# Kernel optimization log

Measured on AMD Instinct MI355X. Metric: run time of the kernel, lower is better.

## Reference

```python
import jax, jax.numpy as jnp
import numpy as np

NUM_HEADS = 16
D_MODEL = 1024
D_K = 64
D_V = 64
NEG_INF = -1e9


def setup_inputs() -> dict:
    key = jax.random.key(0)
    ks = jax.random.split(key, 7)
    B, S = 2, 2048
    Q = jax.random.normal(ks[0], (B, S, D_MODEL), dtype=jnp.float32)
    K = jax.random.normal(ks[1], (B, S, D_MODEL), dtype=jnp.float32)
    V = jax.random.normal(ks[2], (B, S, D_MODEL), dtype=jnp.float32)
    s = 1.0 / np.sqrt(D_MODEL)
    W_q = jax.random.normal(ks[3], (D_MODEL, D_K * NUM_HEADS), dtype=jnp.float32) * s
    W_k = jax.random.normal(ks[4], (D_MODEL, D_K), dtype=jnp.float32) * s
    W_v = jax.random.normal(ks[5], (D_MODEL, D_V), dtype=jnp.float32) * s
    W_o = jax.random.normal(ks[6], (D_V * NUM_HEADS, D_MODEL), dtype=jnp.float32) * (1.0 / np.sqrt(D_V * NUM_HEADS))
    return {"Q": Q, "K": K, "V": V, "W_q": W_q, "W_k": W_k, "W_v": W_v, "W_o": W_o}


def reference(Q, K, V, W_q, W_k, W_v, W_o):
    B, Sq, _ = Q.shape
    Sk = K.shape[1]
    # projections: Q -> per-head, K/V -> single shared head (MQA)
    q = (Q @ W_q).reshape(B, Sq, NUM_HEADS, D_K).transpose(0, 2, 1, 3)  # [B,H,Sq,Dk]
    k = K @ W_k  # [B,Sk,Dk]
    v = V @ W_v  # [B,Sk,Dv]
    scores = jnp.einsum('bhqd,bkd->bhqk', q, k) / jnp.sqrt(jnp.float32(D_K))
    causal = jnp.tril(jnp.ones((Sq, Sk), dtype=bool))  # [Sq,Sk]
    scores = jnp.where(causal[None, None], scores, NEG_INF)
    attn = jax.nn.softmax(scores, axis=-1)  # [B,H,Sq,Sk]
    out = jnp.einsum('bhqk,bkd->bhqd', attn, v)  # [B,H,Sq,Dv]
    out = out.transpose(0, 2, 1, 3).reshape(B, Sq, NUM_HEADS * D_V)
    return out @ W_o
```

## Files before the change

### kernel.cpp

```cpp
#include <hip/hip_runtime.h>
#include <hip/hip_bf16.h>
#include <cstdint>

typedef __bf16 bf16_t;
typedef __bf16 bf16x8 __attribute__((ext_vector_type(8)));
typedef __bf16 bf16x4 __attribute__((ext_vector_type(4)));
typedef float  floatx4 __attribute__((ext_vector_type(4)));

__device__ __forceinline__ bf16_t f2bf(float x) { return (bf16_t)x; }

__device__ __forceinline__ void gll16(const void* g, void* l) {
  __builtin_amdgcn_global_load_lds((const __attribute__((address_space(1))) void*)g,
                                   (__attribute__((address_space(3))) void*)l, 16, 0, 0);
}

#define S_LEN 2048
#define NHEAD 16

__global__ __launch_bounds__(256) void prep_all(const float* __restrict__ Wq,
                                                const float* __restrict__ Wo,
                                                const float* __restrict__ Wk,
                                                const float* __restrict__ Wv,
                                                const float* __restrict__ Q,
                                                bf16_t* __restrict__ Wqt,
                                                bf16_t* __restrict__ Wot,
                                                bf16_t* __restrict__ Wkt,
                                                bf16_t* __restrict__ Wvt,
                                                bf16_t* __restrict__ Qb) {
  const int bid = blockIdx.x;
  if (bid >= 2176) {
    const int base = (bid - 2176) * 8192;
#pragma unroll
    for (int j = 0; j < 8; ++j) {
      int idx = base + j * 1024 + threadIdx.x * 4;
      float4 v = *(const float4*)(Q + idx);
      bf16x4 o;
      o[0] = f2bf(v.x); o[1] = f2bf(v.y); o[2] = f2bf(v.z); o[3] = f2bf(v.w);
      *(bf16x4*)(Qb + idx) = o;
    }
    return;
  }
  const float* W; bf16_t* Wt; int n0, k0, N;
  if (bid < 2048) {
    int z = bid >> 10, rem = bid & 1023;
    W = z ? Wo : Wq; Wt = z ? Wot : Wqt;
    n0 = (rem & 31) * 32; k0 = (rem >> 5) * 32; N = 1024;
  } else {
    int b2 = bid - 2048, z = b2 >> 6, rem = b2 & 63;
    W = z ? Wv : Wk; Wt = z ? Wvt : Wkt;
    n0 = (rem & 1) * 32; k0 = (rem >> 1) * 32; N = 64;
  }
  const int K = 1024;
  __shared__ float tile[32][33];
  int tx = threadIdx.x & 31, ty = threadIdx.x >> 5;
#pragma unroll
  for (int r = 0; r < 4; ++r)
    tile[ty + 8 * r][tx] = W[(size_t)(k0 + ty + 8 * r) * N + n0 + tx];
  __syncthreads();
#pragma unroll
  for (int r = 0; r < 4; ++r)
    Wt[(size_t)(n0 + ty + 8 * r) * K + k0 + tx] = f2bf(tile[tx][ty + 8 * r]);
}

template <int OUTMODE>
__device__ __forceinline__ void gemm64_body(const bf16_t* __restrict__ A,
                                            const bf16_t* __restrict__ Bt,
                                            void* __restrict__ Cout,
                                            int M, int N, int K,
                                            int m0, int n0,
                                            bf16_t* As, bf16_t* Bs) {
  const int tid = threadIdx.x;
  const int wave = tid >> 6, lane = tid & 63;
  const int quad = lane >> 4, lm = lane & 15;
  const int wr = wave >> 1, wc = wave & 1;

  floatx4 acc[2][2];
#pragma unroll
  for (int i = 0; i < 2; ++i)
#pragma unroll
    for (int j = 0; j < 2; ++j) acc[i][j] = (floatx4){0.f, 0.f, 0.f, 0.f};

  for (int k0 = 0; k0 < K; k0 += 64) {
#pragma unroll
    for (int rd = 0; rd < 2; ++rd) {
      int idx = rd * 256 + tid, row = idx >> 3, ch = (idx & 7) ^ (row & 7);
      gll16(A + (size_t)(m0 + row) * K + k0 + ch * 8,
            As + (rd * 256 + wave * 64) * 8);
    }
#pragma unroll
    for (int rd = 0; rd < 2; ++rd) {
      int idx = rd * 256 + tid, row = idx >> 3, ch = (idx & 7) ^ (row & 7);
      gll16(Bt + (size_t)(n0 + row) * K + k0 + ch * 8,
            Bs + (rd * 256 + wave * 64) * 8);
    }
    __syncthreads();
    const int sw = lm & 7;
    bf16x8 af[2][2], bfr[2][2];
#pragma unroll
    for (int i = 0; i < 2; ++i) {
      const bf16_t* base = &As[(wr * 32 + i * 16 + lm) * 64];
      af[i][0] = *(const bf16x8*)(base + ((quad ^ sw) * 8));
      af[i][1] = *(const bf16x8*)(base + (((4 + quad) ^ sw) * 8));
    }
#pragma unroll
    for (int j = 0; j < 2; ++j) {
      const bf16_t* base = &Bs[(wc * 32 + j * 16 + lm) * 64];
      bfr[j][0] = *(const bf16x8*)(base + ((quad ^ sw) * 8));
      bfr[j][1] = *(const bf16x8*)(base + (((4 + quad) ^ sw) * 8));
    }
#pragma unroll
    for (int ks = 0; ks < 2; ++ks)
#pragma unroll
      for (int i = 0; i < 2; ++i)
#pragma unroll
        for (int j = 0; j < 2; ++j)
          acc[i][j] = __builtin_amdgcn_mfma_f32_16x16x32_bf16(af[i][ks], bfr[j][ks],
                                                              acc[i][j], 0, 0, 0);
    __syncthreads();
  }
#pragma unroll
  for (int i = 0; i < 2; ++i) {
#pragma unroll
    for (int j = 0; j < 2; ++j) {
      int row0 = m0 + wr * 32 + i * 16 + quad * 4;
      int col = n0 + wc * 32 + j * 16 + lm;
#pragma unroll
      for (int r = 0; r < 4; ++r) {
        if constexpr (OUTMODE == 3)
          ((bf16_t*)Cout)[(size_t)(row0 + r) * N + col] = f2bf(acc[i][j][r] * 0.125f);
        else
          ((float*)Cout)[(size_t)(row0 + r) * N + col] = acc[i][j][r];
      }
    }
  }
}

__device__ __forceinline__ void kv_body(const float* __restrict__ A32,
                                        const bf16_t* __restrict__ Bt,
                                        bf16_t* __restrict__ kp,
                                        bf16_t* __restrict__ vpt,
                                        int M, int K, int m0, int isV,
                                        bf16_t* As, bf16_t* Bs) {
  constexpr int BK = 32, LDK = 40, N = 64;
  const int tid = threadIdx.x;
  const int wave = tid >> 6, lane = tid & 63;
  const int quad = lane >> 4, lm = lane & 15;
  const int wr = wave >> 1, wc = wave & 1;

  floatx4 acc[2][2];
#pragma unroll
  for (int i = 0; i < 2; ++i)
#pragma unroll
    for (int j = 0; j < 2; ++j) acc[i][j] = (floatx4){0.f, 0.f, 0.f, 0.f};

  for (int k0 = 0; k0 < K; k0 += BK) {
    {
      int row = tid >> 2, c8 = tid & 3;
      const float* src = A32 + (size_t)(m0 + row) * K + k0 + c8 * 8;
      float4 f0 = *(const float4*)src;
      float4 f1 = *(const float4*)(src + 4);
      bf16x8 o;
      o[0] = f2bf(f0.x); o[1] = f2bf(f0.y); o[2] = f2bf(f0.z); o[3] = f2bf(f0.w);
      o[4] = f2bf(f1.x); o[5] = f2bf(f1.y); o[6] = f2bf(f1.z); o[7] = f2bf(f1.w);
      *(bf16x8*)&As[row * LDK + c8 * 8] = o;
    }
    {
      int row = tid >> 2, c8 = tid & 3;
      *(bf16x8*)&Bs[row * LDK + c8 * 8] =
          *(const bf16x8*)(Bt + (size_t)row * K + k0 + c8 * 8);
    }
    __syncthreads();
    bf16x8 af[2], bfr[2];
#pragma unroll
    for (int i = 0; i < 2; ++i)
      af[i] = *(const bf16x8*)&As[(wr * 32 + i * 16 + lm) * LDK + quad * 8];
#pragma unroll
    for (int j = 0; j < 2; ++j)
      bfr[j] = *(const bf16x8*)&Bs[(wc * 32 + j * 16 + lm) * LDK + quad * 8];
#pragma unroll
    for (int i = 0; i < 2; ++i)
#pragma unroll
      for (int j = 0; j < 2; ++j)
        acc[i][j] = __builtin_amdgcn_mfma_f32_16x16x32_bf16(af[i], bfr[j],
                                                            acc[i][j], 0, 0, 0);
    __syncthreads();
  }
#pragma unroll
  for (int i = 0; i < 2; ++i) {
#pragma unroll
    for (int j = 0; j < 2; ++j) {
      int row0 = m0 + wr * 32 + i * 16 + quad * 4;
      int col = wc * 32 + j * 16 + lm;
      if (isV) {
        bf16x4 o;
#pragma unroll
        for (int r = 0; r < 4; ++r) o[r] = f2bf(acc[i][j][r]);
        *(bf16x4*)&vpt[(size_t)col * M + row0] = o;
      } else {
#pragma unroll
        for (int r = 0; r < 4; ++r)
          kp[(size_t)(row0 + r) * N + col] = f2bf(acc[i][j][r]);
      }
    }
  }
}

__global__ __launch_bounds__(256, 4) void proj_all(const bf16_t* __restrict__ Qb,
                                                   const float* __restrict__ K,
                                                   const float* __restrict__ V,
                                                   const bf16_t* __restrict__ Wqt,
                                                   const bf16_t* __restrict__ Wkt,
                                                   const bf16_t* __restrict__ Wvt,
                                                   bf16_t* __restrict__ qp,
                                                   bf16_t* __restrict__ kp,
                                                   bf16_t* __restrict__ vpt,
                                                   int BS) {
  __shared__ __align__(16) bf16_t As[64 * 64];
  __shared__ __align__(16) bf16_t Bs[64 * 64];
  const int bid = blockIdx.x;
  const int mB = BS / 64;
  const int nQ = mB * 16;
  if (bid < nQ) {
    int m0 = (bid % mB) * 64, n0 = (bid / mB) * 64;
    gemm64_body<3>(Qb, Wqt, qp, BS, 1024, 1024, m0, n0, As, Bs);
  } else {
    int b2 = bid - nQ;
    int isV = (b2 >= mB);
    int m0 = (b2 % mB) * 64;
    kv_body(isV ? V : K, isV ? Wvt : Wkt, kp, vpt, BS, 1024, m0, isV, As, Bs);
  }
}

__global__ __launch_bounds__(256, 4) void gemm_oproj(const bf16_t* __restrict__ A,
                                                     const bf16_t* __restrict__ Bt,
                                                     float* __restrict__ Cout,
                                                     int M, int N, int K) {
  __shared__ __align__(16) bf16_t As[64 * 64];
  __shared__ __align__(16) bf16_t Bs[64 * 64];
  gemm64_body<0>(A, Bt, Cout, M, N, K, blockIdx.x * 64, blockIdx.y * 64, As, Bs);
}

__global__ __launch_bounds__(256, 2) void flash_mqa(const bf16_t* __restrict__ q,
                                                    const bf16_t* __restrict__ kk,
                                                    const bf16_t* __restrict__ vt,
                                                    bf16_t* __restrict__ Opart,
                                                    float* __restrict__ lpart,
                                                    int BStot) {
  const int c = blockIdx.x;
  int qt, s;
  if (c < 16)      { qt = c; s = 0; }
  else if (c < 48) { qt = 16 + ((c - 16) >> 1); s = (c - 16) & 1; }
  else if (c < 96) { int d = c - 48; int q3 = d / 3; qt = 32 + q3; s = d - q3 * 3; }
  else             { qt = 48 + ((c - 96) >> 2); s = (c - 96) & 3; }
  const int n = (qt >> 1) + 1;
  const int nchunks = (n + 7) >> 3;
  const int kt0 = s * 8;
  const int kt1 = (kt0 + 8 < n) ? kt0 + 8 : n;
  const int ktmax = n - 1;

  const int hg = blockIdx.y, b = blockIdx.z;
  const int tid = threadIdx.x;
  const int wave = tid >> 6, lane = tid & 63;
  const int quad = lane >> 4, lm = lane & 15;
  const int h = hg * 4 + wave;

  __shared__ __align__(16) bf16_t k_lds[2][64 * 64];
  __shared__ __align__(16) bf16_t v_lds[2][64 * 64];
  __shared__ __align__(16) bf16_t p_lds[4][32 * 64];

  const size_t bS = (size_t)b * S_LEN;
  const int qb = qt * 32;
  const int qoff = qb - ktmax * 64;
  const int sw = lm & 7;

  bf16x8 qf[2][2];
#pragma unroll
  for (int m = 0; m < 2; ++m) {
    const bf16_t* qp = q + (bS + qb + m * 16 + lm) * 1024 + h * 64;
    qf[m][0] = *(const bf16x8*)(qp + quad * 8);
    qf[m][1] = *(const bf16x8*)(qp + 32 + quad * 8);
  }
  bf16x8 onesf;
#pragma unroll
  for (int j = 0; j < 8; ++j) onesf[j] = f2bf(1.0f);

  floatx4 acc[2][4];
  floatx4 ps[2];
#pragma unroll
  for (int m = 0; m < 2; ++m) {
    ps[m] = (floatx4){0.f, 0.f, 0.f, 0.f};
#pragma unroll
    for (int t = 0; t < 4; ++t) acc[m][t] = (floatx4){0.f, 0.f, 0.f, 0.f};
  }

  bf16x8 kst[2], vst[2];
  auto load_kv = [&](int kt) {
    const int k0 = kt * 64;
#pragma unroll
    for (int it = 0; it < 2; ++it) {
      int idx = it * 256 + tid, r = idx >> 3, c8 = idx & 7;
      kst[it] = *(const bf16x8*)(kk + (bS + k0 + r) * 64 + c8 * 8);
      vst[it] = *(const bf16x8*)(vt + (size_t)r * BStot + bS + k0 + c8 * 8);
    }
  };
  auto write_kv = [&](int buf) {
#pragma unroll
    for (int it = 0; it < 2; ++it) {
      int idx = it * 256 + tid, r = idx >> 3, c8 = idx & 7;
      int addr = r * 64 + ((c8 ^ (r & 7)) * 8);
      *(bf16x8*)&k_lds[buf][addr] = kst[it];
      *(bf16x8*)&v_lds[buf][addr] = vst[it];
    }
  };

  load_kv(kt0);
  write_kv(kt0 & 1);
  __syncthreads();

  for (int kt = kt0; kt < kt1; ++kt) {
    const int cur = kt & 1;
    if (kt + 1 < kt1) load_kv(kt + 1);
    const bool diag = (kt == ktmax);

#pragma unroll
    for (int t = 0; t < 4; ++t) {
      const bf16_t* kb = &k_lds[cur][(t * 16 + lm) * 64];
      bf16x8 a0 = *(const bf16x8*)(kb + ((quad ^ sw) * 8));
      bf16x8 a1 = *(const bf16x8*)(kb + (((4 + quad) ^ sw) * 8));
      floatx4 sv[2];
#pragma unroll
      for (int m = 0; m < 2; ++m) {
        floatx4 cc = (floatx4){0.f, 0.f, 0.f, 0.f};
        cc = __builtin_amdgcn_mfma_f32_16x16x32_bf16(a0, qf[m][0], cc, 0, 0, 0);
        cc = __builtin_amdgcn_mfma_f32_16x16x32_bf16(a1, qf[m][1], cc, 0, 0, 0);
        sv[m] = cc;
      }
      if (diag) {
#pragma unroll
        for (int m = 0; m < 2; ++m) {
          int qq = qoff + m * 16 + lm;
#pragma unroll
          for (int r = 0; r < 4; ++r) {
            int kj = t * 16 + quad * 4 + r;
            sv[m][r] = (kj <= qq) ? __expf(sv[m][r]) : 0.f;
          }
        }
      } else {
#pragma unroll
        for (int m = 0; m < 2; ++m)
#pragma unroll
          for (int r = 0; r < 4; ++r) sv[m][r] = __expf(sv[m][r]);
      }
#pragma unroll
      for (int m = 0; m < 2; ++m) {
        bf16x4 pk;
#pragma unroll
        for (int r = 0; r < 4; ++r) pk[r] = f2bf(sv[m][r]);
        *(bf16x4*)&p_lds[wave][(m * 16 + lm) * 64 +
                               (((2 * t + (quad >> 1)) ^ sw) * 8) + (quad & 1) * 4] = pk;
      }
    }
    bf16x8 p0[2], p1[2];
#pragma unroll
    for (int m = 0; m < 2; ++m) {
      const bf16_t* pb = &p_lds[wave][(m * 16 + lm) * 64];
      p0[m] = *(const bf16x8*)(pb + ((quad ^ sw) * 8));
      p1[m] = *(const bf16x8*)(pb + (((4 + quad) ^ sw) * 8));
      ps[m] = __builtin_amdgcn_mfma_f32_16x16x32_bf16(p0[m], onesf, ps[m], 0, 0, 0);
      ps[m] = __builtin_amdgcn_mfma_f32_16x16x32_bf16(p1[m], onesf, ps[m], 0, 0, 0);
    }
#pragma unroll
    for (int t = 0; t < 4; ++t) {
      const bf16_t* vb = &v_lds[cur][(t * 16 + lm) * 64];
      bf16x8 v0 = *(const bf16x8*)(vb + ((quad ^ sw) * 8));
      bf16x8 v1 = *(const bf16x8*)(vb + (((4 + quad) ^ sw) * 8));
#pragma unroll
      for (int m = 0; m < 2; ++m) {
        acc[m][t] = __builtin_amdgcn_mfma_f32_16x16x32_bf16(p0[m], v0, acc[m][t], 0, 0, 0);
        acc[m][t] = __builtin_amdgcn_mfma_f32_16x16x32_bf16(p1[m], v1, acc[m][t], 0, 0, 0);
      }
    }
    if (kt + 1 < kt1) write_kv(1 - cur);
    __syncthreads();
  }

  const size_t slotO = (size_t)BStot * 1024;
  const size_t slotL = (size_t)BStot * 16;
#pragma unroll
  for (int m = 0; m < 2; ++m) {
    const int q0 = qb + m * 16 + quad * 4;
#pragma unroll
    for (int t = 0; t < 4; ++t)
#pragma unroll
      for (int r = 0; r < 4; ++r)
        Opart[s * slotO + (bS + q0 + r) * 1024 + h * 64 + t * 16 + lm] =
            f2bf(acc[m][t][r]);
    if (lm == 0)
#pragma unroll
      for (int r = 0; r < 4; ++r)
        lpart[s * slotL + (bS + q0 + r) * 16 + h] = ps[m][r];
  }
  if (s == 0) {
    for (int ss = nchunks; ss < 4; ++ss) {
#pragma unroll
      for (int m = 0; m < 2; ++m) {
        const int q0 = qb + m * 16 + quad * 4;
#pragma unroll
        for (int t = 0; t < 4; ++t)
#pragma unroll
          for (int r = 0; r < 4; ++r)
            Opart[ss * slotO + (bS + q0 + r) * 1024 + h * 64 + t * 16 + lm] = f2bf(0.f);
        if (lm == 0)
#pragma unroll
          for (int r = 0; r < 4; ++r)
            lpart[ss * slotL + (bS + q0 + r) * 16 + h] = 0.f;
      }
    }
  }
}

__global__ __launch_bounds__(256) void combine_o(const bf16_t* __restrict__ Opart,
                                                 const float* __restrict__ lpart,
                                                 bf16_t* __restrict__ Ob, int BS) {
  const int idx = (blockIdx.x * 256 + threadIdx.x) * 8;
  const int row = idx >> 10, col = idx & 1023, h = col >> 6;
  const size_t slotO = (size_t)BS * 1024;
  const size_t slotL = (size_t)BS * 16;
  float l = 0.f;
#pragma unroll
  for (int s = 0; s < 4; ++s) l += lpart[s * slotL + row * 16 + h];
  float o[8];
#pragma unroll
  for (int j = 0; j < 8; ++j) o[j] = 0.f;
#pragma unroll
  for (int s = 0; s < 4; ++s) {
    bf16x8 v = *(const bf16x8*)(Opart + s * slotO + idx);
#pragma unroll
    for (int j = 0; j < 8; ++j) o[j] += (float)v[j];
  }
  const float rl = 1.0f / l;
  bf16x8 out;
#pragma unroll
  for (int j = 0; j < 8; ++j) out[j] = f2bf(o[j] * rl);
  *(bf16x8*)(Ob + idx) = out;
}

extern "C" void kernel_launch(void* const* d_in, const int* in_sizes, int n_in,
                              void* d_out, int out_size, void* d_ws, size_t ws_size,
                              hipStream_t stream) {
  const float* Q  = (const float*)d_in[0];
  const float* K  = (const float*)d_in[1];
  const float* V  = (const float*)d_in[2];
  const float* Wq = (const float*)d_in[3];
  const float* Wk = (const float*)d_in[4];
  const float* Wv = (const float*)d_in[5];
  const float* Wo = (const float*)d_in[6];

  const int BS = in_sizes[0] / 1024;
  const int B  = BS / S_LEN;

  bf16_t* ws  = (bf16_t*)d_ws;
  bf16_t* qp  = ws;
  bf16_t* Ob  = qp  + (size_t)BS * 1024;
  bf16_t* Wqt = Ob  + (size_t)BS * 1024;
  bf16_t* Wot = Wqt + (size_t)1024 * 1024;
  bf16_t* Wkt = Wot + (size_t)1024 * 1024;
  bf16_t* Wvt = Wkt + (size_t)64 * 1024;
  bf16_t* kp  = Wvt + (size_t)64 * 1024;
  bf16_t* vpt = kp  + (size_t)BS * 64;
  bf16_t* Opart = vpt + (size_t)BS * 64;
  float*  lpart = (float*)(Opart + (size_t)4 * BS * 1024);
  bf16_t* Qb  = (bf16_t*)(lpart + (size_t)4 * BS * 16);

  prep_all<<<2176 + BS / 8, 256, 0, stream>>>(Wq, Wo, Wk, Wv, Q,
                                              Wqt, Wot, Wkt, Wvt, Qb);

  proj_all<<<(BS / 64) * 16 + (BS / 64) * 2, 256, 0, stream>>>(
      Qb, K, V, Wqt, Wkt, Wvt, qp, kp, vpt, BS);

  flash_mqa<<<dim3(160, NHEAD / 4, B), 256, 0, stream>>>(qp, kp, vpt, Opart, lpart, BS);

  combine_o<<<(BS * 1024) / (256 * 8), 256, 0, stream>>>(Opart, lpart, Ob, BS);

  gemm_oproj<<<dim3(BS / 64, 16), 256, 0, stream>>>(Ob, Wot, (float*)d_out, BS, 1024, 1024);
}
```

Before: 194.0 us.

## Double-buffer GEMM tiles through registers and widen N tile to 128

```diff
diff --git a/kernel.cpp b/kernel.cpp
--- a/kernel.cpp
+++ b/kernel.cpp
@@ -8,11 +8,6 @@
 typedef float  floatx4 __attribute__((ext_vector_type(4)));
 
 __device__ __forceinline__ bf16_t f2bf(float x) { return (bf16_t)x; }
-
-__device__ __forceinline__ void gll16(const void* g, void* l) {
-  __builtin_amdgcn_global_load_lds((const __attribute__((address_space(1))) void*)g,
-                                   (__attribute__((address_space(3))) void*)l, 16, 0, 0);
-}
 
 #define S_LEN 2048
 #define NHEAD 16
@@ -63,48 +58,72 @@
 }
 
 template <int OUTMODE>
-__device__ __forceinline__ void gemm64_body(const bf16_t* __restrict__ A,
-                                            const bf16_t* __restrict__ Bt,
-                                            void* __restrict__ Cout,
-                                            int M, int N, int K,
-                                            int m0, int n0,
-                                            bf16_t* As, bf16_t* Bs) {
+__device__ __forceinline__ void gemm_body(const bf16_t* __restrict__ A,
+                                          const bf16_t* __restrict__ Bt,
+                                          void* __restrict__ Cout,
+                                          int M, int N, int K,
+                                          int m0, int n0,
+                                          bf16_t* As, bf16_t* Bs) {
   const int tid = threadIdx.x;
   const int wave = tid >> 6, lane = tid & 63;
   const int quad = lane >> 4, lm = lane & 15;
   const int wr = wave >> 1, wc = wave & 1;
-
-  floatx4 acc[2][2];
+  const int sw = lm & 7;
+
+  floatx4 acc[2][4];
 #pragma unroll
   for (int i = 0; i < 2; ++i)
 #pragma unroll
-    for (int j = 0; j < 2; ++j) acc[i][j] = (floatx4){0.f, 0.f, 0.f, 0.f};
-
-  for (int k0 = 0; k0 < K; k0 += 64) {
+    for (int j = 0; j < 4; ++j) acc[i][j] = (floatx4){0.f, 0.f, 0.f, 0.f};
+
+  const int nIter = K / 64;
+  const int phase = blockIdx.x & (nIter - 1);
+
+  bf16x8 ast[2], bst[4];
+  auto load_t = [&](int it) {
+    const int kk = ((it + phase) & (nIter - 1)) * 64;
 #pragma unroll
     for (int rd = 0; rd < 2; ++rd) {
-      int idx = rd * 256 + tid, row = idx >> 3, ch = (idx & 7) ^ (row & 7);
-      gll16(A + (size_t)(m0 + row) * K + k0 + ch * 8,
-            As + (rd * 256 + wave * 64) * 8);
-    }
+      int idx = rd * 256 + tid, row = idx >> 3, c8 = idx & 7;
+      ast[rd] = *(const bf16x8*)(A + (size_t)(m0 + row) * K + kk + c8 * 8);
+    }
+#pragma unroll
+    for (int rd = 0; rd < 4; ++rd) {
+      int idx = rd * 256 + tid, row = idx >> 3, c8 = idx & 7;
+      bst[rd] = *(const bf16x8*)(Bt + (size_t)(n0 + row) * K + kk + c8 * 8);
+    }
+  };
+  auto write_t = [&](int buf) {
 #pragma unroll
     for (int rd = 0; rd < 2; ++rd) {
-      int idx = rd * 256 + tid, row = idx >> 3, ch = (idx & 7) ^ (row & 7);
-      gll16(Bt + (size_t)(n0 + row) * K + k0 + ch * 8,
-            Bs + (rd * 256 + wave * 64) * 8);
-    }
-    __syncthreads();
-    const int sw = lm & 7;
-    bf16x8 af[2][2], bfr[2][2];
+      int idx = rd * 256 + tid, row = idx >> 3, c8 = idx & 7;
+      *(bf16x8*)&As[buf * 4096 + row * 64 + ((c8 ^ (row & 7)) * 8)] = ast[rd];
+    }
+#pragma unroll
+    for (int rd = 0; rd < 4; ++rd) {
+      int idx = rd * 256 + tid, row = idx >> 3, c8 = idx & 7;
+      *(bf16x8*)&Bs[buf * 8192 + row * 64 + ((c8 ^ (row & 7)) * 8)] = bst[rd];
+    }
+  };
+
+  load_t(0);
+  write_t(0);
+  __syncthreads();
+
+  for (int it = 0; it < nIter; ++it) {
+    const int cur = it & 1;
+    if (it + 1 < nIter) load_t(it + 1);
+
+    bf16x8 af[2][2], bfr[4][2];
 #pragma unroll
     for (int i = 0; i < 2; ++i) {
-      const bf16_t* base = &As[(wr * 32 + i * 16 + lm) * 64];
+      const bf16_t* base = &As[cur * 4096 + (wr * 32 + i * 16 + lm) * 64];
       af[i][0] = *(const bf16x8*)(base + ((quad ^ sw) * 8));
       af[i][1] = *(const bf16x8*)(base + (((4 + quad) ^ sw) * 8));
     }
 #pragma unroll
-    for (int j = 0; j < 2; ++j) {
-      const bf16_t* base = &Bs[(wc * 32 + j * 16 + lm) * 64];
+    for (int j = 0; j < 4; ++j) {
+      const bf16_t* base = &Bs[cur * 8192 + (wc * 64 + j * 16 + lm) * 64];
       bfr[j][0] = *(const bf16x8*)(base + ((quad ^ sw) * 8));
       bfr[j][1] = *(const bf16x8*)(base + (((4 + quad) ^ sw) * 8));
     }
@@ -113,17 +132,19 @@
 #pragma unroll
       for (int i = 0; i < 2; ++i)
 #pragma unroll
-        for (int j = 0; j < 2; ++j)
+        for (int j = 0; j < 4; ++j)
           acc[i][j] = __builtin_amdgcn_mfma_f32_16x16x32_bf16(af[i][ks], bfr[j][ks],
                                                               acc[i][j], 0, 0, 0);
+    if (it + 1 < nIter) write_t(1 - cur);
     __syncthreads();
   }
+
 #pragma unroll
   for (int i = 0; i < 2; ++i) {
 #pragma unroll
-    for (int j = 0; j < 2; ++j) {
+    for (int j = 0; j < 4; ++j) {
       int row0 = m0 + wr * 32 + i * 16 + quad * 4;
-      int col = n0 + wc * 32 + j * 16 + lm;
+      int col = n0 + wc * 64 + j * 16 + lm;
 #pragma unroll
       for (int r = 0; r < 4; ++r) {
         if constexpr (OUTMODE == 3)
@@ -205,7 +226,7 @@
   }
 }
 
-__global__ __launch_bounds__(256, 4) void proj_all(const bf16_t* __restrict__ Qb,
+__global__ __launch_bounds__(256, 3) void proj_all(const bf16_t* __restrict__ Qb,
                                                    const float* __restrict__ K,
                                                    const float* __restrict__ V,
                                                    const bf16_t* __restrict__ Wqt,
@@ -215,14 +236,14 @@
                                                    bf16_t* __restrict__ kp,
                                                    bf16_t* __restrict__ vpt,
                                                    int BS) {
-  __shared__ __align__(16) bf16_t As[64 * 64];
-  __shared__ __align__(16) bf16_t Bs[64 * 64];
+  __shared__ __align__(16) bf16_t As[2 * 64 * 64];
+  __shared__ __align__(16) bf16_t Bs[2 * 128 * 64];
   const int bid = blockIdx.x;
   const int mB = BS / 64;
-  const int nQ = mB * 16;
+  const int nQ = mB * 8;
   if (bid < nQ) {
-    int m0 = (bid % mB) * 64, n0 = (bid / mB) * 64;
-    gemm64_body<3>(Qb, Wqt, qp, BS, 1024, 1024, m0, n0, As, Bs);
+    int m0 = (bid % mB) * 64, n0 = (bid / mB) * 128;
+    gemm_body<3>(Qb, Wqt, qp, BS, 1024, 1024, m0, n0, As, Bs);
   } else {
     int b2 = bid - nQ;
     int isV = (b2 >= mB);
@@ -231,13 +252,13 @@
   }
 }
 
-__global__ __launch_bounds__(256, 4) void gemm_oproj(const bf16_t* __restrict__ A,
+__global__ __launch_bounds__(256, 3) void gemm_oproj(const bf16_t* __restrict__ A,
                                                      const bf16_t* __restrict__ Bt,
                                                      float* __restrict__ Cout,
                                                      int M, int N, int K) {
-  __shared__ __align__(16) bf16_t As[64 * 64];
-  __shared__ __align__(16) bf16_t Bs[64 * 64];
-  gemm64_body<0>(A, Bt, Cout, M, N, K, blockIdx.x * 64, blockIdx.y * 64, As, Bs);
+  __shared__ __align__(16) bf16_t As[2 * 64 * 64];
+  __shared__ __align__(16) bf16_t Bs[2 * 128 * 64];
+  gemm_body<0>(A, Bt, Cout, M, N, K, blockIdx.x * 64, blockIdx.y * 128, As, Bs);
 }
 
 __global__ __launch_bounds__(256, 2) void flash_mqa(const bf16_t* __restrict__ q,
@@ -475,12 +496,12 @@
   prep_all<<<2176 + BS / 8, 256, 0, stream>>>(Wq, Wo, Wk, Wv, Q,
                                               Wqt, Wot, Wkt, Wvt, Qb);
 
-  proj_all<<<(BS / 64) * 16 + (BS / 64) * 2, 256, 0, stream>>>(
+  proj_all<<<(BS / 64) * 8 + (BS / 64) * 2, 256, 0, stream>>>(
       Qb, K, V, Wqt, Wkt, Wvt, qp, kp, vpt, BS);
 
   flash_mqa<<<dim3(160, NHEAD / 4, B), 256, 0, stream>>>(qp, kp, vpt, Opart, lpart, BS);
 
   combine_o<<<(BS * 1024) / (256 * 8), 256, 0, stream>>>(Opart, lpart, Ob, BS);
 
-  gemm_oproj<<<dim3(BS / 64, 16), 256, 0, stream>>>(Ob, Wot, (float*)d_out, BS, 1024, 1024);
-}
+  gemm_oproj<<<dim3(BS / 64, 8), 256, 0, stream>>>(Ob, Wot, (float*)d_out, BS, 1024, 1024);
+}
```

Result: no change. 193.2 us (-0.4%).
